# Kernel tuning notes

Measured on AMD Instinct MI355X. Metric: run time of the kernel, lower is better.

Reference implementation:

```python
import jax, jax.numpy as jnp
import numpy as np


def _chamfer(samp_pc, ref_pc):
    """Squared-L2 chamfer: returns (cost_p1_p2 [B,N], cost_p2_p1 [B,M]).

    samp_pc: [B, N, 3], ref_pc: [B, M, 3]
    """
    s2 = jnp.sum(samp_pc * samp_pc, axis=-1)  # [B, N]
    r2 = jnp.sum(ref_pc * ref_pc, axis=-1)    # [B, M]
    cross = jnp.einsum('bnd,bmd->bnm', samp_pc, ref_pc)  # [B, N, M]
    d2 = s2[:, :, None] + r2[:, None, :] - 2.0 * cross   # [B, N, M]
    d2 = jnp.maximum(d2, 0.0)  # numerical floor
    cost_p1_p2 = jnp.min(d2, axis=2)  # [B, N] nearest ref for each samp point
    cost_p2_p1 = jnp.min(d2, axis=1)  # [B, M] nearest samp for each ref point
    return cost_p1_p2, cost_p2_p1


def setup_inputs() -> dict:
    key = jax.random.key(0)
    k1, k2 = jax.random.split(key)
    B, N, M = 16, 2048, 8192
    ref_pc = jax.random.normal(k1, (B, M, 3), dtype=jnp.float32)
    samp_pc = jax.random.normal(k2, (B, N, 3), dtype=jnp.float32)
    return {"ref_pc": ref_pc, "samp_pc": samp_pc}


def reference(ref_pc, samp_pc):
    cost_p1_p2, cost_p2_p1 = _chamfer(samp_pc, ref_pc)
    cd_p = (jnp.sqrt(cost_p1_p2).mean(axis=1) + jnp.sqrt(cost_p2_p1).mean(axis=1)) / 2.0
    cd_t = cost_p1_p2.mean(axis=1) + cost_p2_p1.mean(axis=1)
    return (cd_p, cd_t)
```

## Files before the change

### kernel.cpp

```cpp
#include <hip/hip_runtime.h>
#include <math.h>

#define BB 16
#define NN 2048
#define MM 8192

#define BLK 256
#define R 8
#define G (BLK * R)
#define YS (MM / G)
#define QCH 32
#define ZS (NN / QCH)
#define QPH 16
#define PHASES (QCH / QPH)

typedef float v2f __attribute__((ext_vector_type(2)));

static __device__ __forceinline__ v2f v2_splat(float s) { v2f r; r.x = s; r.y = s; return r; }
static __device__ __forceinline__ v2f v2_fma(v2f a, v2f b, v2f c) {
#if __has_builtin(__builtin_elementwise_fma)
    return __builtin_elementwise_fma(a, b, c);
#else
    v2f r; r.x = fmaf(a.x, b.x, c.x); r.y = fmaf(a.y, b.y, c.y); return r;
#endif
}


__global__ void __launch_bounds__(BLK, 4) sweep_kernel(const float* __restrict__ ref,
                                                       const float* __restrict__ samp,
                                                       unsigned int* __restrict__ ws2,
                                                       unsigned int* __restrict__ ws1) {
    __shared__ v2f tqbuf[(QPH / 2) * BLK];
    __shared__ float4 qbuf[QCH];

    const int b = blockIdx.x;
    const int lane = threadIdx.x & 63;
    const int wv = threadIdx.x >> 6;
    const int refbase = blockIdx.y * G + wv * (64 * R);
    const int q0 = blockIdx.z * QCH;

    if (threadIdx.x < QCH / 2) {
        const int k = threadIdx.x;
        const float* s0 = samp + ((size_t)b * NN + q0 + 2 * k) * 3;
        float x0 = s0[0], y0 = s0[1], z0 = s0[2];
        float x1 = s0[3], y1 = s0[4], z1 = s0[5];
        float w0 = fmaf(x0, x0, fmaf(y0, y0, z0 * z0));
        float w1 = fmaf(x1, x1, fmaf(y1, y1, z1 * z1));
        qbuf[2 * k]     = make_float4(x0, x1, y0, y1);
        qbuf[2 * k + 1] = make_float4(z0, z1, w0, w1);
    }

    const float* rp = ref + ((size_t)b * MM + refbase) * 3;
    float px[R], py[R], pz[R], pp[R], mref[R];
#pragma unroll
    for (int r = 0; r < R; ++r) {
        const float* pq = rp + (size_t)(r * 64 + lane) * 3;
        float p1 = pq[0], p2 = pq[1], p3 = pq[2];
        pp[r] = fmaf(p1, p1, fmaf(p2, p2, p3 * p3));
        px[r] = -2.f * p1; py[r] = -2.f * p2; pz[r] = -2.f * p3;
        mref[r] = INFINITY;
    }
    __syncthreads();

    unsigned int* w1 = ws1 + (size_t)b * NN + q0;

    for (int ph = 0; ph < PHASES; ++ph) {
#pragma unroll 2
        for (int j = 0; j < QPH / 2; ++j) {
            const int jp = ph * (QPH / 2) + j;
            float4 a = qbuf[2 * jp];
            float4 c = qbuf[2 * jp + 1];
            v2f qx; qx.x = a.x; qx.y = a.y;
            v2f qy; qy.x = a.z; qy.y = a.w;
            v2f qz; qz.x = c.x; qz.y = c.y;
            v2f qw; qw.x = c.z; qw.y = c.w;
            v2f t[R];
#pragma unroll
            for (int r = 0; r < R; ++r) {
                v2f s = v2_fma(v2_splat(px[r]), qx, v2_splat(pp[r]));
                s = v2_fma(v2_splat(py[r]), qy, s);
                s = v2_fma(v2_splat(pz[r]), qz, s);
                t[r] = s + qw;
            }
#pragma unroll
            for (int r = 0; r < R; ++r)
                mref[r] = fminf(fminf(mref[r], t[r].x), t[r].y);
            v2f o;
            {
                float a0 = fminf(t[0].x, t[1].x), a1 = fminf(t[2].x, t[3].x);
                float a2 = fminf(t[4].x, t[5].x), a3 = fminf(t[6].x, t[7].x);
                o.x = fminf(fminf(a0, a1), fminf(a2, a3));
                float b0 = fminf(t[0].y, t[1].y), b1 = fminf(t[2].y, t[3].y);
                float b2 = fminf(t[4].y, t[5].y), b3 = fminf(t[6].y, t[7].y);
                o.y = fminf(fminf(b0, b1), fminf(b2, b3));
            }
            tqbuf[j * BLK + threadIdx.x] = o;
        }
        __syncthreads();

#pragma unroll
        for (int jj = 0; jj < (QPH / 2) / 4; ++jj) {
            const int jp = wv * ((QPH / 2) / 4) + jj;
            const v2f* s2 = tqbuf + jp * BLK;
            v2f v0 = s2[lane], v1 = s2[lane + 64], v2_ = s2[lane + 128], v3 = s2[lane + 192];
            float m0 = fminf(fminf(v0.x, v1.x), fminf(v2_.x, v3.x));
            float m1 = fminf(fminf(v0.y, v1.y), fminf(v2_.y, v3.y));
#pragma unroll
            for (int s = 32; s > 0; s >>= 1) {
                m0 = fminf(m0, __shfl_xor(m0, s));
                m1 = fminf(m1, __shfl_xor(m1, s));
            }
            if (lane == 0) {
                atomicMin(&w1[ph * QPH + 2 * jp],     __float_as_uint(fmaxf(m0, 0.f)));
                atomicMin(&w1[ph * QPH + 2 * jp + 1], __float_as_uint(fmaxf(m1, 0.f)));
            }
        }
        __syncthreads();
    }

    unsigned int* w2 = ws2 + (size_t)b * MM + refbase;
#pragma unroll
    for (int r = 0; r < R; ++r)
        atomicMin(&w2[r * 64 + lane], __float_as_uint(fmaxf(mref[r], 0.f)));
}

#define BLKR 1024
__global__ void __launch_bounds__(BLKR) reduce_kernel(const unsigned int* __restrict__ ws1,
                                                      const unsigned int* __restrict__ ws2,
                                                      float* __restrict__ out) {
    const int b = blockIdx.x;
    const int tid = threadIdx.x;
    const int lane = tid & 63;
    const int wv = tid >> 6;

    float sd1 = 0.f, sr1 = 0.f, sd2 = 0.f, sr2 = 0.f;
#pragma unroll
    for (int i = tid; i < NN; i += BLKR) {
        float v = __uint_as_float(ws1[(size_t)b * NN + i]);
        sd1 += v;
        sr1 += sqrtf(v);
    }
#pragma unroll
    for (int i = tid; i < MM; i += BLKR) {
        float v = __uint_as_float(ws2[(size_t)b * MM + i]);
        sd2 += v;
        sr2 += sqrtf(v);
    }
#pragma unroll
    for (int s = 32; s > 0; s >>= 1) {
        sd1 += __shfl_xor(sd1, s);
        sr1 += __shfl_xor(sr1, s);
        sd2 += __shfl_xor(sd2, s);
        sr2 += __shfl_xor(sr2, s);
    }

    __shared__ float4 red[BLKR / 64];
    if (lane == 0) red[wv] = make_float4(sd1, sr1, sd2, sr2);
    __syncthreads();
    if (tid == 0) {
        float4 acc = red[0];
#pragma unroll
        for (int w = 1; w < BLKR / 64; ++w) {
            acc.x += red[w].x; acc.y += red[w].y;
            acc.z += red[w].z; acc.w += red[w].w;
        }
        out[b]      = (acc.y * (1.0f / NN) + acc.w * (1.0f / MM)) * 0.5f;
        out[BB + b] = acc.x * (1.0f / NN) + acc.z * (1.0f / MM);
    }
}

extern "C" void kernel_launch(void* const* d_in, const int* in_sizes, int n_in,
                              void* d_out, int out_size, void* d_ws, size_t ws_size,
                              hipStream_t stream) {
    const float* ref  = (const float*)d_in[0];
    const float* samp = (const float*)d_in[1];
    float* out = (float*)d_out;

    unsigned int* ws2 = (unsigned int*)d_ws;
    unsigned int* ws1 = ws2 + (size_t)BB * MM;

    hipMemsetAsync(d_ws, 0x7F, ((size_t)BB * MM + (size_t)BB * NN) * sizeof(unsigned int), stream);

    dim3 gs(BB, YS, ZS);
    sweep_kernel<<<gs, BLK, 0, stream>>>(ref, samp, ws2, ws1);

    reduce_kernel<<<BB, BLKR, 0, stream>>>(ws1, ws2, out);
}
```

Before: 106.8 us.

## Compute chamfer distances with bf16x3-split MFMA and a packing prep kernel

Adds a prep kernel that writes each point and each reference point as a 5-term augmented vector (coordinates, squared norm, constant 1). Each term is split into three bf16 pieces and packed into 32-wide K operands, with the B rows written in a swizzled order. The sweep kernel then gets the full distance expression from 16x16x32 bf16 MFMA instructions in place of scalar packed-FMA code, then does min-reductions and atomics. This moves the bulk of the arithmetic onto matrix units. It adds an extra kernel launch, workspace traffic, and a precision risk, since the 6-term bf16 split drops the lowest-order cross products.

```diff
diff --git a/kernel.cpp b/kernel.cpp
--- a/kernel.cpp
+++ b/kernel.cpp
@@ -5,123 +5,167 @@
 #define NN 2048
 #define MM 8192
 
+#define TN 128
+#define TM 512
 #define BLK 256
-#define R 8
-#define G (BLK * R)
-#define YS (MM / G)
-#define QCH 32
-#define ZS (NN / QCH)
-#define QPH 16
-#define PHASES (QCH / QPH)
-
-typedef float v2f __attribute__((ext_vector_type(2)));
-
-static __device__ __forceinline__ v2f v2_splat(float s) { v2f r; r.x = s; r.y = s; return r; }
-static __device__ __forceinline__ v2f v2_fma(v2f a, v2f b, v2f c) {
-#if __has_builtin(__builtin_elementwise_fma)
-    return __builtin_elementwise_fma(a, b, c);
-#else
-    v2f r; r.x = fmaf(a.x, b.x, c.x); r.y = fmaf(a.y, b.y, c.y); return r;
-#endif
-}
-
-
-__global__ void __launch_bounds__(BLK, 4) sweep_kernel(const float* __restrict__ ref,
-                                                       const float* __restrict__ samp,
+
+typedef __attribute__((ext_vector_type(8))) short short8;
+typedef __attribute__((ext_vector_type(4))) float f32x4;
+
+union U16 { uint4 u; short8 s; };
+
+static __device__ __forceinline__ unsigned short f2bf(float f) {
+    unsigned int u = __float_as_uint(f);
+    unsigned int r = (u + 0x7FFFu + ((u >> 16) & 1u)) >> 16;
+    return (unsigned short)r;
+}
+static __device__ __forceinline__ float bf2f(unsigned short h) {
+    return __uint_as_float(((unsigned int)h) << 16);
+}
+
+
+__global__ void __launch_bounds__(BLK) prep_kernel(const float* __restrict__ ref,
+                                                   const float* __restrict__ samp,
+                                                   unsigned short* __restrict__ Apk,
+                                                   unsigned short* __restrict__ Bpk) {
+    const int i = blockIdx.x * BLK + threadIdx.x;
+    const int PN = BB * NN;
+    float a5[5];
+    unsigned short h[3][5];
+    unsigned short K[32];
+
+    if (i < PN) {
+        const float* s0 = samp + (size_t)i * 3;
+        float x = s0[0], y = s0[1], z = s0[2];
+        a5[0] = x; a5[1] = y; a5[2] = z;
+        a5[3] = fmaf(x, x, fmaf(y, y, z * z)); a5[4] = 1.f;
+#pragma unroll
+        for (int j = 0; j < 5; ++j) {
+            float v = a5[j];
+            h[0][j] = f2bf(v); float r1 = v - bf2f(h[0][j]);
+            h[1][j] = f2bf(r1); float r2 = r1 - bf2f(h[1][j]);
+            h[2][j] = f2bf(r2);
+        }
+        const int ordA[6] = {0, 0, 1, 0, 2, 1};
+#pragma unroll
+        for (int t = 0; t < 6; ++t)
+#pragma unroll
+            for (int j = 0; j < 5; ++j) K[t * 5 + j] = h[ordA[t]][j];
+        K[30] = 0; K[31] = 0;
+        unsigned int uu[16];
+#pragma unroll
+        for (int t = 0; t < 16; ++t)
+            uu[t] = (unsigned int)K[2 * t] | ((unsigned int)K[2 * t + 1] << 16);
+        uint4* dst = (uint4*)(Apk + (size_t)i * 32);
+        dst[0] = make_uint4(uu[0], uu[1], uu[2], uu[3]);
+        dst[1] = make_uint4(uu[4], uu[5], uu[6], uu[7]);
+        dst[2] = make_uint4(uu[8], uu[9], uu[10], uu[11]);
+        dst[3] = make_uint4(uu[12], uu[13], uu[14], uu[15]);
+    } else if (i < PN + BB * MM) {
+        const int j = i - PN;
+        const int m = j & (MM - 1);
+        const float* r0 = ref + (size_t)j * 3;
+        float x = r0[0], y = r0[1], z = r0[2];
+        a5[0] = -2.f * x; a5[1] = -2.f * y; a5[2] = -2.f * z;
+        a5[3] = 1.f; a5[4] = fmaf(x, x, fmaf(y, y, z * z));
+#pragma unroll
+        for (int jj = 0; jj < 5; ++jj) {
+            float v = a5[jj];
+            h[0][jj] = f2bf(v); float r1 = v - bf2f(h[0][jj]);
+            h[1][jj] = f2bf(r1); float r2 = r1 - bf2f(h[1][jj]);
+            h[2][jj] = f2bf(r2);
+        }
+        const int ordB[6] = {0, 1, 0, 2, 0, 1};
+#pragma unroll
+        for (int t = 0; t < 6; ++t)
+#pragma unroll
+            for (int jj = 0; jj < 5; ++jj) K[t * 5 + jj] = h[ordB[t]][jj];
+        K[30] = 0; K[31] = 0;
+        unsigned int uu[16];
+#pragma unroll
+        for (int t = 0; t < 16; ++t)
+            uu[t] = (unsigned int)K[2 * t] | ((unsigned int)K[2 * t + 1] << 16);
+        uint4 c0 = make_uint4(uu[0], uu[1], uu[2], uu[3]);
+        uint4 c1 = make_uint4(uu[4], uu[5], uu[6], uu[7]);
+        uint4 c2 = make_uint4(uu[8], uu[9], uu[10], uu[11]);
+        uint4 c3 = make_uint4(uu[12], uu[13], uu[14], uu[15]);
+        uint4* dst = (uint4*)(Bpk + (size_t)j * 32);
+        const int s = (m >> 1) & 3;
+        dst[0 ^ s] = c0; dst[1 ^ s] = c1; dst[2 ^ s] = c2; dst[3 ^ s] = c3;
+    }
+}
+
+__global__ void __launch_bounds__(BLK, 4) sweep_kernel(const unsigned short* __restrict__ Apk,
+                                                       const unsigned short* __restrict__ Bpk,
                                                        unsigned int* __restrict__ ws2,
                                                        unsigned int* __restrict__ ws1) {
-    __shared__ v2f tqbuf[(QPH / 2) * BLK];
-    __shared__ float4 qbuf[QCH];
+    __shared__ uint4 Bt[TM * 4];
 
     const int b = blockIdx.x;
-    const int lane = threadIdx.x & 63;
-    const int wv = threadIdx.x >> 6;
-    const int refbase = blockIdx.y * G + wv * (64 * R);
-    const int q0 = blockIdx.z * QCH;
-
-    if (threadIdx.x < QCH / 2) {
-        const int k = threadIdx.x;
-        const float* s0 = samp + ((size_t)b * NN + q0 + 2 * k) * 3;
-        float x0 = s0[0], y0 = s0[1], z0 = s0[2];
-        float x1 = s0[3], y1 = s0[4], z1 = s0[5];
-        float w0 = fmaf(x0, x0, fmaf(y0, y0, z0 * z0));
-        float w1 = fmaf(x1, x1, fmaf(y1, y1, z1 * z1));
-        qbuf[2 * k]     = make_float4(x0, x1, y0, y1);
-        qbuf[2 * k + 1] = make_float4(z0, z1, w0, w1);
-    }
-
-    const float* rp = ref + ((size_t)b * MM + refbase) * 3;
-    float px[R], py[R], pz[R], pp[R], mref[R];
-#pragma unroll
-    for (int r = 0; r < R; ++r) {
-        const float* pq = rp + (size_t)(r * 64 + lane) * 3;
-        float p1 = pq[0], p2 = pq[1], p3 = pq[2];
-        pp[r] = fmaf(p1, p1, fmaf(p2, p2, p3 * p3));
-        px[r] = -2.f * p1; py[r] = -2.f * p2; pz[r] = -2.f * p3;
-        mref[r] = INFINITY;
-    }
+    const int n0 = blockIdx.y * TN;
+    const int m0 = blockIdx.z * TM;
+    const int tid = threadIdx.x;
+    const int w = tid >> 6;
+    const int l = tid & 63;
+    const int r = l & 15;
+    const int g = l >> 4;
+
+    const uint4* bs = (const uint4*)(Bpk + ((size_t)(b * MM + m0)) * 32);
+#pragma unroll
+    for (int k = 0; k < (TM * 4) / BLK; ++k) Bt[tid + k * BLK] = bs[tid + k * BLK];
+
+    const uint4* ap = (const uint4*)(Apk + ((size_t)(b * NN + n0 + w * 32)) * 32);
+    U16 a0, a1;
+    a0.u = ap[(r << 2) + g];
+    a1.u = ap[64 + (r << 2) + g];
     __syncthreads();
 
-    unsigned int* w1 = ws1 + (size_t)b * NN + q0;
-
-    for (int ph = 0; ph < PHASES; ++ph) {
-#pragma unroll 2
-        for (int j = 0; j < QPH / 2; ++j) {
-            const int jp = ph * (QPH / 2) + j;
-            float4 a = qbuf[2 * jp];
-            float4 c = qbuf[2 * jp + 1];
-            v2f qx; qx.x = a.x; qx.y = a.y;
-            v2f qy; qy.x = a.z; qy.y = a.w;
-            v2f qz; qz.x = c.x; qz.y = c.y;
-            v2f qw; qw.x = c.z; qw.y = c.w;
-            v2f t[R];
-#pragma unroll
-            for (int r = 0; r < R; ++r) {
-                v2f s = v2_fma(v2_splat(px[r]), qx, v2_splat(pp[r]));
-                s = v2_fma(v2_splat(py[r]), qy, s);
-                s = v2_fma(v2_splat(pz[r]), qz, s);
-                t[r] = s + qw;
-            }
-#pragma unroll
-            for (int r = 0; r < R; ++r)
-                mref[r] = fminf(fminf(mref[r], t[r].x), t[r].y);
-            v2f o;
-            {
-                float a0 = fminf(t[0].x, t[1].x), a1 = fminf(t[2].x, t[3].x);
-                float a2 = fminf(t[4].x, t[5].x), a3 = fminf(t[6].x, t[7].x);
-                o.x = fminf(fminf(a0, a1), fminf(a2, a3));
-                float b0 = fminf(t[0].y, t[1].y), b1 = fminf(t[2].y, t[3].y);
-                float b2 = fminf(t[4].y, t[5].y), b3 = fminf(t[6].y, t[7].y);
-                o.y = fminf(fminf(b0, b1), fminf(b2, b3));
-            }
-            tqbuf[j * BLK + threadIdx.x] = o;
-        }
-        __syncthreads();
-
-#pragma unroll
-        for (int jj = 0; jj < (QPH / 2) / 4; ++jj) {
-            const int jp = wv * ((QPH / 2) / 4) + jj;
-            const v2f* s2 = tqbuf + jp * BLK;
-            v2f v0 = s2[lane], v1 = s2[lane + 64], v2_ = s2[lane + 128], v3 = s2[lane + 192];
-            float m0 = fminf(fminf(v0.x, v1.x), fminf(v2_.x, v3.x));
-            float m1 = fminf(fminf(v0.y, v1.y), fminf(v2_.y, v3.y));
-#pragma unroll
-            for (int s = 32; s > 0; s >>= 1) {
-                m0 = fminf(m0, __shfl_xor(m0, s));
-                m1 = fminf(m1, __shfl_xor(m1, s));
-            }
-            if (lane == 0) {
-                atomicMin(&w1[ph * QPH + 2 * jp],     __float_as_uint(fmaxf(m0, 0.f)));
-                atomicMin(&w1[ph * QPH + 2 * jp + 1], __float_as_uint(fmaxf(m1, 0.f)));
-            }
-        }
-        __syncthreads();
-    }
-
-    unsigned int* w2 = ws2 + (size_t)b * MM + refbase;
-#pragma unroll
-    for (int r = 0; r < R; ++r)
-        atomicMin(&w2[r * 64 + lane], __float_as_uint(fmaxf(mref[r], 0.f)));
+    float qa0 = INFINITY, qa1 = INFINITY, qa2 = INFINITY, qa3 = INFINITY;
+    float qb0 = INFINITY, qb1 = INFINITY, qb2 = INFINITY, qb3 = INFINITY;
+
+    const uint4* bp = Bt + (r << 2) + (g ^ ((r >> 1) & 3));
+    unsigned int* w2 = ws2 + (size_t)b * MM + m0;
+    const f32x4 fz = {0.f, 0.f, 0.f, 0.f};
+
+#pragma unroll 4
+    for (int ct = 0; ct < TM / 16; ++ct) {
+        U16 bu; bu.u = bp[ct * 64];
+        f32x4 d0 = __builtin_amdgcn_mfma_f32_16x16x32_bf16(a0.s, bu.s, fz, 0, 0, 0);
+        f32x4 d1 = __builtin_amdgcn_mfma_f32_16x16x32_bf16(a1.s, bu.s, fz, 0, 0, 0);
+        qa0 = fminf(qa0, d0[0]); qa1 = fminf(qa1, d0[1]);
+        qa2 = fminf(qa2, d0[2]); qa3 = fminf(qa3, d0[3]);
+        qb0 = fminf(qb0, d1[0]); qb1 = fminf(qb1, d1[1]);
+        qb2 = fminf(qb2, d1[2]); qb3 = fminf(qb3, d1[3]);
+        float rm = fminf(fminf(fminf(d0[0], d0[1]), fminf(d0[2], d0[3])),
+                         fminf(fminf(d1[0], d1[1]), fminf(d1[2], d1[3])));
+        rm = fminf(rm, __shfl_xor(rm, 16));
+        rm = fminf(rm, __shfl_xor(rm, 32));
+        if (g == 0)
+            atomicMin(&w2[ct * 16 + r], __float_as_uint(fmaxf(rm, 0.f)));
+    }
+
+#pragma unroll
+    for (int s = 1; s <= 8; s <<= 1) {
+        qa0 = fminf(qa0, __shfl_xor(qa0, s));
+        qa1 = fminf(qa1, __shfl_xor(qa1, s));
+        qa2 = fminf(qa2, __shfl_xor(qa2, s));
+        qa3 = fminf(qa3, __shfl_xor(qa3, s));
+        qb0 = fminf(qb0, __shfl_xor(qb0, s));
+        qb1 = fminf(qb1, __shfl_xor(qb1, s));
+        qb2 = fminf(qb2, __shfl_xor(qb2, s));
+        qb3 = fminf(qb3, __shfl_xor(qb3, s));
+    }
+    if (r == 0) {
+        unsigned int* w1 = ws1 + (size_t)b * NN + n0 + w * 32 + g * 4;
+        atomicMin(&w1[0],  __float_as_uint(fmaxf(qa0, 0.f)));
+        atomicMin(&w1[1],  __float_as_uint(fmaxf(qa1, 0.f)));
+        atomicMin(&w1[2],  __float_as_uint(fmaxf(qa2, 0.f)));
+        atomicMin(&w1[3],  __float_as_uint(fmaxf(qa3, 0.f)));
+        atomicMin(&w1[16], __float_as_uint(fmaxf(qb0, 0.f)));
+        atomicMin(&w1[17], __float_as_uint(fmaxf(qb1, 0.f)));
+        atomicMin(&w1[18], __float_as_uint(fmaxf(qb2, 0.f)));
+        atomicMin(&w1[19], __float_as_uint(fmaxf(qb3, 0.f)));
+    }
 }
 
 #define BLKR 1024
@@ -178,11 +222,16 @@
 
     unsigned int* ws2 = (unsigned int*)d_ws;
     unsigned int* ws1 = ws2 + (size_t)BB * MM;
+    unsigned short* Apk = (unsigned short*)(ws1 + (size_t)BB * NN);
+    unsigned short* Bpk = Apk + (size_t)BB * NN * 32;
 
     hipMemsetAsync(d_ws, 0x7F, ((size_t)BB * MM + (size_t)BB * NN) * sizeof(unsigned int), stream);
 
-    dim3 gs(BB, YS, ZS);
-    sweep_kernel<<<gs, BLK, 0, stream>>>(ref, samp, ws2, ws1);
+    const int P = BB * (NN + MM);
+    prep_kernel<<<P / BLK, BLK, 0, stream>>>(ref, samp, Apk, Bpk);
+
+    dim3 gs(BB, NN / TN, MM / TM);
+    sweep_kernel<<<gs, BLK, 0, stream>>>(Apk, Bpk, ws2, ws1);
 
     reduce_kernel<<<BB, BLKR, 0, stream>>>(ws1, ws2, out);
 }
```

Result: slower. 170.3 us (+59.5%).
